# Kernel optimization log

Measured on AMD Instinct MI355X. Metric: run time of the kernel, lower is better.

## Reference

```python
import jax, jax.numpy as jnp
import numpy as np

B, N, K, C = 4, 4096, 32, 192  # batch, npoint, nsample, channels (C % 6 == 0)
EPS = 1e-5


def setup_inputs() -> dict:
    key = jax.random.key(0)
    ks = jax.random.split(key, 8)
    p = jax.random.normal(ks[0], (B, N, 3), jnp.float32)
    x = jax.random.normal(ks[1], (B, C, N), jnp.float32)
    idx = jax.random.randint(ks[2], (B, N, K), 0, N)  # ball-query neighbor ids
    W = jax.random.normal(ks[3], (C, C + 3), jnp.float32) * 0.05  # 1x1 conv weight
    gamma = 1.0 + 0.1 * jax.random.normal(ks[4], (C,), jnp.float32)
    beta = 0.1 * jax.random.normal(ks[5], (C,), jnp.float32)
    rmean = 0.1 * jax.random.normal(ks[6], (C,), jnp.float32)
    rvar = jax.random.uniform(ks[7], (C,), jnp.float32) + 0.5  # positive running var
    return dict(p=p, x=x, idx=idx, W=W, gamma=gamma, beta=beta, rmean=rmean, rvar=rvar)


def reference(p, x, idx, W, gamma, beta, rmean, rvar):
    # --- grouper: gather neighbors, relative coords ---
    pn = jax.vmap(lambda pp, ii: pp[ii])(p, idx)            # [B,N,K,3]
    dp = jnp.transpose(pn - p[:, :, None, :], (0, 3, 1, 2))  # [B,3,N,K]
    xj = jax.vmap(lambda xx, ii: xx[:, ii])(x, idx)          # [B,C,N,K]
    # --- PosPool sin/cos positional embedding fused with features ---
    feat_dim = C // 6
    dim_mat = jnp.power(500.0, jnp.arange(feat_dim, dtype=jnp.float32) / feat_dim)
    div = (50.0 * dp)[..., None] / dim_mat                   # [B,3,N,K,fd]
    pe = jnp.concatenate([jnp.sin(div), jnp.cos(div)], axis=-1)  # [B,3,N,K,2fd]
    pe = jnp.transpose(pe, (0, 1, 4, 2, 3)).reshape(B, C, N, K)  # [B,C,N,K]
    agg = xj * pe + pe
    # --- dp_fj concat -> 1x1 conv -> BN(eval) -> ReLU ---
    h = jnp.concatenate([dp, agg], axis=1)                   # [B,C+3,N,K]
    y = jnp.einsum('oc,bcnk->bonk', W, h)                    # [B,C,N,K]
    inv = gamma / jnp.sqrt(rvar + EPS)
    y = y * inv[:, None, None] + (beta - rmean * inv)[:, None, None]
    y = jax.nn.relu(y)
    # --- max reduction over neighbors ---
    return jnp.max(y, axis=-1)                               # [B,C,N]
```

## Files before the change

kernel.cpp:

```cpp
#include <hip/hip_runtime.h>
#include <math.h>

#define B_   4
#define N_   4096
#define K_   32
#define C_   192
#define CH_  195
#define KPAD 224
#define NKT6 6
#define NNT8 8
#define GRID 512

using half8  = __attribute__((ext_vector_type(8))) _Float16;
using half2v = __attribute__((ext_vector_type(2))) _Float16;
using f32x4  = __attribute__((ext_vector_type(4))) float;

__device__ _Float16 g_Wp[C_ * KPAD];
__device__ _Float16 g_xT[(size_t)B_ * N_ * C_];

__global__ __launch_bounds__(256) void prep(const float* __restrict__ x,
                                            const float* __restrict__ W,
                                            const float* __restrict__ gamma_,
                                            const float* __restrict__ rvar) {
    const int tid = threadIdx.x;
    if (blockIdx.x < 512) {
        __shared__ float s[32][201];
        const int b  = blockIdx.x >> 7;
        const int n0 = (blockIdx.x & 127) * 32;
        const int cl = tid >> 3;
        const int n4 = (tid & 7) * 4;
#pragma unroll
        for (int it = 0; it < 6; ++it) {
            const int c = it * 32 + cl;
            const float4 v = *(const float4*)(x + ((size_t)b * C_ + c) * N_ + n0 + n4);
            s[n4 + 0][c] = v.x; s[n4 + 1][c] = v.y; s[n4 + 2][c] = v.z; s[n4 + 3][c] = v.w;
        }
        __syncthreads();
        const int n  = tid >> 3;
        const int og = tid & 7;
#pragma unroll
        for (int it = 0; it < 3; ++it) {
            const int oc = it * 8 + og;
            half8 v;
#pragma unroll
            for (int jj = 0; jj < 8; ++jj) v[jj] = (_Float16)s[n][oc * 8 + jj];
            *(half8*)(g_xT + ((size_t)b * N_ + n0 + n) * C_ + oc * 8) = v;
        }
    } else {
        const int i = (blockIdx.x - 512) * 256 + tid;
        if (i < C_ * KPAD) {
            const int o = i / KPAD, r = i - o * KPAD;
            const float inv = gamma_[o] * rsqrtf(rvar[o] + 1e-5f);
            float v = 0.0f;
            if (r < 192)      v = W[o * CH_ + 3 + r];
            else if (r < 195) v = W[o * CH_ + (r - 192)];
            g_Wp[i] = (_Float16)(v * inv);
        }
    }
}

__global__ __launch_bounds__(256, 2) void la_mfma(
    const float* __restrict__ p,
    const int*   __restrict__ idx,
    const float* __restrict__ gamma_,
    const float* __restrict__ beta_,
    const float* __restrict__ rmean,
    const float* __restrict__ rvar,
    float* __restrict__ out)
{
    __shared__ _Float16 hb[NKT6 * NNT8 * 64 * 8];
    __shared__ float s_d[3][128];
    __shared__ float s_bias[C_], s_fr[32];

    const int tid  = threadIdx.x;
    const int lane = tid & 63;
    const int w    = tid >> 6;
    const int l15  = lane & 15;
    const int quad = lane >> 4;

    const int xcd      = blockIdx.x & 7;
    const int slot     = blockIdx.x >> 3;
    const int pairbase = xcd * 1024 + slot * 16;
    const int iters    = 8;
    const int b        = xcd >> 1;

    if (tid < C_) {
        const float inv = gamma_[tid] * rsqrtf(rvar[tid] + 1e-5f);
        s_bias[tid] = beta_[tid] - rmean[tid] * inv;
    }
    if (tid < 32) s_fr[tid] = 7.9577471546f * exp2f(-(float)tid * 0.2801808715263400f);
    __syncthreads();

    float sfr[8];
#pragma unroll
    for (int jj = 0; jj < 8; ++jj) sfr[jj] = s_fr[quad * 8 + jj];

    const int pt = w >> 1;
    const int k  = (w & 1) * 16 + l15;

    int j0 = idx[(size_t)((pairbase + 0) * 2 + pt) * K_ + k];
    int j1 = idx[(size_t)((pairbase + 1) * 2 + pt) * K_ + k];

    for (int it = 0; it < iters; ++it) {
        const int pr0 = pairbase + 2 * it;
        const int n0  = (pr0 * 2) & (N_ - 1);

#pragma unroll
        for (int pp = 0; pp < 2; ++pp) {
            const int j  = pp ? j1 : j0;
            const int gp = (pr0 + pp) * 2 + pt;
            const float d0 = p[(size_t)(b * N_ + j) * 3 + 0] - p[(size_t)gp * 3 + 0];
            const float d1 = p[(size_t)(b * N_ + j) * 3 + 1] - p[(size_t)gp * 3 + 1];
            const float d2 = p[(size_t)(b * N_ + j) * 3 + 2] - p[(size_t)gp * 3 + 2];
            const _Float16* xh = g_xT + ((size_t)b * N_ + j) * C_;
            const int nt = pp * 4 + w;

#pragma unroll
            for (int i6 = 0; i6 < 6; ++i6) {
                const int chunk = quad + 4 * i6;
                const half8 v = *(const half8*)(xh + chunk * 8);
                const float dd  = (chunk < 8) ? d0 : ((chunk < 16) ? d1 : d2);
                const float off = (chunk & 4) ? 0.25f : 0.0f;
                half8 hv;
#pragma unroll
                for (int jj = 0; jj < 8; jj += 2) {
                    const float pe0 = __builtin_amdgcn_sinf(fmaf(dd, sfr[jj],     off));
                    const float pe1 = __builtin_amdgcn_sinf(fmaf(dd, sfr[jj + 1], off));
                    const half2v pe2 = __builtin_bit_cast(half2v, __builtin_amdgcn_cvt_pkrtz(pe0, pe1));
                    half2v v2; v2[0] = v[jj]; v2[1] = v[jj + 1];
                    const half2v r2 = pe2 * v2 + pe2;
                    hv[jj] = r2[0]; hv[jj + 1] = r2[1];
                }
                *(half8*)(&hb[(size_t)((i6 * NNT8 + nt) * 64 + quad * 16 + l15) * 8]) = hv;
            }
            if (quad == 0) {
                const int col = nt * 16 + l15;
                s_d[0][col] = d0; s_d[1][col] = d1; s_d[2][col] = d2;
            }
        }
        __syncthreads();

        if (it + 1 < iters) {
            j0 = idx[(size_t)((pr0 + 2) * 2 + pt) * K_ + k];
            j1 = idx[(size_t)((pr0 + 3) * 2 + pt) * K_ + k];
        }

        f32x4 acc[3][8];
#pragma unroll
        for (int i = 0; i < 3; ++i)
#pragma unroll
            for (int t = 0; t < 8; ++t) acc[i][t] = (f32x4)0.0f;

#pragma unroll
        for (int kt = 0; kt < NKT6; ++kt) {
            const int k0 = kt * 32 + quad * 8;
            half8 a[3];
#pragma unroll
            for (int i = 0; i < 3; ++i)
                a[i] = *(const half8*)(g_Wp + (size_t)((w * 3 + i) * 16 + l15) * KPAD + k0);
#pragma unroll
            for (int t = 0; t < 8; ++t) {
                const half8 bf = *(const half8*)(&hb[(size_t)((kt * NNT8 + t) * 64 + lane) * 8]);
#pragma unroll
                for (int i = 0; i < 3; ++i)
                    acc[i][t] = __builtin_amdgcn_mfma_f32_16x16x32_f16(bf, a[i], acc[i][t], 0, 0, 0);
            }
        }
        {
            half8 a6[3];
#pragma unroll
            for (int i = 0; i < 3; ++i)
                a6[i] = *(const half8*)(g_Wp + (size_t)((w * 3 + i) * 16 + l15) * KPAD + 6 * 32 + quad * 8);
#pragma unroll
            for (int t = 0; t < 8; ++t) {
                const int col = t * 16 + l15;
                half8 b6 = (half8)(_Float16)0.0f;
                const float e0 = s_d[0][col];
                const float e1 = s_d[1][col];
                const float e2 = s_d[2][col];
                if (quad == 0) {
                    b6[0] = (_Float16)e0; b6[1] = (_Float16)e1; b6[2] = (_Float16)e2;
                }
#pragma unroll
                for (int i = 0; i < 3; ++i)
                    acc[i][t] = __builtin_amdgcn_mfma_f32_16x16x32_f16(b6, a6[i], acc[i][t], 0, 0, 0);
            }
        }

#pragma unroll
        for (int i = 0; i < 3; ++i) {
            const int m = (w * 3 + i) * 16 + l15;
            float4 o4;
            float ov[4];
#pragma unroll
            for (int pp = 0; pp < 2; ++pp)
#pragma unroll
                for (int ptc = 0; ptc < 2; ++ptc) {
                    const f32x4 va = acc[i][pp * 4 + 2 * ptc];
                    const f32x4 vb = acc[i][pp * 4 + 2 * ptc + 1];
                    float v = fmaxf(fmaxf(fmaxf(va[0], va[1]), fmaxf(va[2], va[3])),
                                    fmaxf(fmaxf(vb[0], vb[1]), fmaxf(vb[2], vb[3])));
                    v = fmaxf(v, __shfl_xor(v, 16, 64));
                    v = fmaxf(v, __shfl_xor(v, 32, 64));
                    ov[pp * 2 + ptc] = v;
                }
            if (quad == 0) {
                const float bias = s_bias[m];
                o4.x = fmaxf(ov[0] + bias, 0.0f);
                o4.y = fmaxf(ov[1] + bias, 0.0f);
                o4.z = fmaxf(ov[2] + bias, 0.0f);
                o4.w = fmaxf(ov[3] + bias, 0.0f);
                *(float4*)(&out[((size_t)b * C_ + m) * N_ + n0]) = o4;
            }
        }
        __syncthreads();
    }
}

extern "C" void kernel_launch(void* const* d_in, const int* in_sizes, int n_in,
                              void* d_out, int out_size, void* d_ws, size_t ws_size,
                              hipStream_t stream) {
    (void)in_sizes; (void)n_in; (void)out_size; (void)d_ws; (void)ws_size;
    const float* p      = (const float*)d_in[0];
    const float* x      = (const float*)d_in[1];
    const int*   idx    = (const int*)d_in[2];
    const float* W      = (const float*)d_in[3];
    const float* gamma_ = (const float*)d_in[4];
    const float* beta_  = (const float*)d_in[5];
    const float* rmean  = (const float*)d_in[6];
    const float* rvar   = (const float*)d_in[7];
    float* out = (float*)d_out;

    prep<<<512 + (C_ * KPAD + 255) / 256, 256, 0, stream>>>(x, W, gamma_, rvar);
    la_mfma<<<GRID, 256, 0, stream>>>(p, idx, gamma_, beta_, rmean, rvar, out);
}
```

Before: 149.1 us.

## Double block size to 512 threads and stage outputs in LDS for wider stores

Each block now uses 8 waves over 8 points per iteration (16 N-tiles), with the grid halved to 256 blocks. Waves split into row groups and tile halves, so each weight fragment load serves the same number of MFMAs per wave but the block covers twice the points. Results are staged in a shared s_out buffer across two iterations and then written as 16 contiguous floats per channel row, replacing scattered 4-float stores. This costs more LDS, an extra barrier per iteration, and fewer blocks, which may lower occupancy and latency hiding.

```diff
diff --git a/kernel.cpp b/kernel.cpp
--- a/kernel.cpp
+++ b/kernel.cpp
@@ -8,8 +8,8 @@
 #define CH_  195
 #define KPAD 224
 #define NKT6 6
-#define NNT8 8
-#define GRID 512
+#define NNT16 16
+#define GRID 256
 
 using half8  = __attribute__((ext_vector_type(8))) _Float16;
 using half2v = __attribute__((ext_vector_type(2))) _Float16;
@@ -59,7 +59,7 @@
     }
 }
 
-__global__ __launch_bounds__(256, 2) void la_mfma(
+__global__ __launch_bounds__(512, 2) void la_mfma(
     const float* __restrict__ p,
     const int*   __restrict__ idx,
     const float* __restrict__ gamma_,
@@ -68,8 +68,9 @@
     const float* __restrict__ rvar,
     float* __restrict__ out)
 {
-    __shared__ _Float16 hb[NKT6 * NNT8 * 64 * 8];
-    __shared__ float s_d[3][128];
+    __shared__ _Float16 hb[7 * NNT16 * 64 * 8];
+    __shared__ float s_d[3][256];
+    __shared__ float s_out[C_][16];
     __shared__ float s_bias[C_], s_fr[32];
 
     const int tid  = threadIdx.x;
@@ -80,7 +81,7 @@
 
     const int xcd      = blockIdx.x & 7;
     const int slot     = blockIdx.x >> 3;
-    const int pairbase = xcd * 1024 + slot * 16;
+    const int pairbase = xcd * 1024 + slot * 32;
     const int iters    = 8;
     const int b        = xcd >> 1;
 
@@ -95,26 +96,22 @@
 #pragma unroll
     for (int jj = 0; jj < 8; ++jj) sfr[jj] = s_fr[quad * 8 + jj];
 
-    const int pt = w >> 1;
-    const int k  = (w & 1) * 16 + l15;
-
-    int j0 = idx[(size_t)((pairbase + 0) * 2 + pt) * K_ + k];
-    int j1 = idx[(size_t)((pairbase + 1) * 2 + pt) * K_ + k];
+    const int k0v = (w & 1) * 16 + l15;
+    const int pp0 = w >> 2,        pt0 = (w >> 1) & 1;
+    const int pp1 = (8 + w) >> 2,  pt1 = ((8 + w) >> 1) & 1;
+
+    int j0 = idx[(size_t)((pairbase + pp0) * 2 + pt0) * K_ + k0v];
+    int j1 = idx[(size_t)((pairbase + pp1) * 2 + pt1) * K_ + k0v];
 
     for (int it = 0; it < iters; ++it) {
-        const int pr0 = pairbase + 2 * it;
-        const int n0  = (pr0 * 2) & (N_ - 1);
-
-#pragma unroll
-        for (int pp = 0; pp < 2; ++pp) {
-            const int j  = pp ? j1 : j0;
+        const int pr0 = pairbase + 4 * it;
+
+        auto build = [&](int T, int jv, int pp, int pt) {
             const int gp = (pr0 + pp) * 2 + pt;
-            const float d0 = p[(size_t)(b * N_ + j) * 3 + 0] - p[(size_t)gp * 3 + 0];
-            const float d1 = p[(size_t)(b * N_ + j) * 3 + 1] - p[(size_t)gp * 3 + 1];
-            const float d2 = p[(size_t)(b * N_ + j) * 3 + 2] - p[(size_t)gp * 3 + 2];
-            const _Float16* xh = g_xT + ((size_t)b * N_ + j) * C_;
-            const int nt = pp * 4 + w;
-
+            const float d0 = p[(size_t)(b * N_ + jv) * 3 + 0] - p[(size_t)gp * 3 + 0];
+            const float d1 = p[(size_t)(b * N_ + jv) * 3 + 1] - p[(size_t)gp * 3 + 1];
+            const float d2 = p[(size_t)(b * N_ + jv) * 3 + 2] - p[(size_t)gp * 3 + 2];
+            const _Float16* xh = g_xT + ((size_t)b * N_ + jv) * C_;
 #pragma unroll
             for (int i6 = 0; i6 < 6; ++i6) {
                 const int chunk = quad + 4 * i6;
@@ -131,20 +128,25 @@
                     const half2v r2 = pe2 * v2 + pe2;
                     hv[jj] = r2[0]; hv[jj + 1] = r2[1];
                 }
-                *(half8*)(&hb[(size_t)((i6 * NNT8 + nt) * 64 + quad * 16 + l15) * 8]) = hv;
+                *(half8*)(&hb[(size_t)((i6 * NNT16 + T) * 64 + quad * 16 + l15) * 8]) = hv;
             }
             if (quad == 0) {
-                const int col = nt * 16 + l15;
+                const int col = T * 16 + l15;
                 s_d[0][col] = d0; s_d[1][col] = d1; s_d[2][col] = d2;
             }
-        }
+        };
+        build(w,     j0, pp0, pt0);
+        build(8 + w, j1, pp1, pt1);
         __syncthreads();
 
+        int jn0 = j0, jn1 = j1;
         if (it + 1 < iters) {
-            j0 = idx[(size_t)((pr0 + 2) * 2 + pt) * K_ + k];
-            j1 = idx[(size_t)((pr0 + 3) * 2 + pt) * K_ + k];
-        }
-
+            jn0 = idx[(size_t)((pr0 + 4 + pp0) * 2 + pt0) * K_ + k0v];
+            jn1 = idx[(size_t)((pr0 + 4 + pp1) * 2 + pt1) * K_ + k0v];
+        }
+
+        const int rg = (w & 3) * 3;
+        const int tb = (w >> 2) * 8;
         f32x4 acc[3][8];
 #pragma unroll
         for (int i = 0; i < 3; ++i)
@@ -153,27 +155,27 @@
 
 #pragma unroll
         for (int kt = 0; kt < NKT6; ++kt) {
-            const int k0 = kt * 32 + quad * 8;
+            const int kk0 = kt * 32 + quad * 8;
             half8 a[3];
 #pragma unroll
             for (int i = 0; i < 3; ++i)
-                a[i] = *(const half8*)(g_Wp + (size_t)((w * 3 + i) * 16 + l15) * KPAD + k0);
-#pragma unroll
-            for (int t = 0; t < 8; ++t) {
-                const half8 bf = *(const half8*)(&hb[(size_t)((kt * NNT8 + t) * 64 + lane) * 8]);
+                a[i] = *(const half8*)(g_Wp + (size_t)((rg + i) * 16 + l15) * KPAD + kk0);
+#pragma unroll
+            for (int tt = 0; tt < 8; ++tt) {
+                const half8 bf = *(const half8*)(&hb[(size_t)((kt * NNT16 + tb + tt) * 64 + lane) * 8]);
 #pragma unroll
                 for (int i = 0; i < 3; ++i)
-                    acc[i][t] = __builtin_amdgcn_mfma_f32_16x16x32_f16(bf, a[i], acc[i][t], 0, 0, 0);
+                    acc[i][tt] = __builtin_amdgcn_mfma_f32_16x16x32_f16(bf, a[i], acc[i][tt], 0, 0, 0);
             }
         }
         {
             half8 a6[3];
 #pragma unroll
             for (int i = 0; i < 3; ++i)
-                a6[i] = *(const half8*)(g_Wp + (size_t)((w * 3 + i) * 16 + l15) * KPAD + 6 * 32 + quad * 8);
-#pragma unroll
-            for (int t = 0; t < 8; ++t) {
-                const int col = t * 16 + l15;
+                a6[i] = *(const half8*)(g_Wp + (size_t)((rg + i) * 16 + l15) * KPAD + 6 * 32 + quad * 8);
+#pragma unroll
+            for (int tt = 0; tt < 8; ++tt) {
+                const int col = (tb + tt) * 16 + l15;
                 half8 b6 = (half8)(_Float16)0.0f;
                 const float e0 = s_d[0][col];
                 const float e1 = s_d[1][col];
@@ -183,37 +185,42 @@
                 }
 #pragma unroll
                 for (int i = 0; i < 3; ++i)
-                    acc[i][t] = __builtin_amdgcn_mfma_f32_16x16x32_f16(b6, a6[i], acc[i][t], 0, 0, 0);
-            }
-        }
-
+                    acc[i][tt] = __builtin_amdgcn_mfma_f32_16x16x32_f16(b6, a6[i], acc[i][tt], 0, 0, 0);
+            }
+        }
+
+        const int pbase = (it & 1) * 8 + (w >> 2) * 4;
 #pragma unroll
         for (int i = 0; i < 3; ++i) {
-            const int m = (w * 3 + i) * 16 + l15;
-            float4 o4;
-            float ov[4];
-#pragma unroll
-            for (int pp = 0; pp < 2; ++pp)
-#pragma unroll
-                for (int ptc = 0; ptc < 2; ++ptc) {
-                    const f32x4 va = acc[i][pp * 4 + 2 * ptc];
-                    const f32x4 vb = acc[i][pp * 4 + 2 * ptc + 1];
-                    float v = fmaxf(fmaxf(fmaxf(va[0], va[1]), fmaxf(va[2], va[3])),
-                                    fmaxf(fmaxf(vb[0], vb[1]), fmaxf(vb[2], vb[3])));
-                    v = fmaxf(v, __shfl_xor(v, 16, 64));
-                    v = fmaxf(v, __shfl_xor(v, 32, 64));
-                    ov[pp * 2 + ptc] = v;
+            const int m = (rg + i) * 16 + l15;
+#pragma unroll
+            for (int qq = 0; qq < 4; ++qq) {
+                const f32x4 va = acc[i][2 * qq];
+                const f32x4 vb = acc[i][2 * qq + 1];
+                float v = fmaxf(fmaxf(fmaxf(va[0], va[1]), fmaxf(va[2], va[3])),
+                                fmaxf(fmaxf(vb[0], vb[1]), fmaxf(vb[2], vb[3])));
+                v = fmaxf(v, __shfl_xor(v, 16, 64));
+                v = fmaxf(v, __shfl_xor(v, 32, 64));
+                if (quad == 0)
+                    s_out[m][pbase + qq] = fmaxf(v + s_bias[m], 0.0f);
+            }
+        }
+        __syncthreads();
+
+        if (it & 1) {
+            const int n0w = ((pr0 - 4) * 2) & (N_ - 1);
+#pragma unroll
+            for (int ss = 0; ss < 2; ++ss) {
+                const int t = ss * 512 + tid;
+                if (t < C_ * 4) {
+                    const int row = t >> 2, c4 = (t & 3) * 4;
+                    const float4 o4 = *(const float4*)(&s_out[row][c4]);
+                    *(float4*)(&out[((size_t)b * C_ + row) * N_ + n0w + c4]) = o4;
                 }
-            if (quad == 0) {
-                const float bias = s_bias[m];
-                o4.x = fmaxf(ov[0] + bias, 0.0f);
-                o4.y = fmaxf(ov[1] + bias, 0.0f);
-                o4.z = fmaxf(ov[2] + bias, 0.0f);
-                o4.w = fmaxf(ov[3] + bias, 0.0f);
-                *(float4*)(&out[((size_t)b * C_ + m) * N_ + n0]) = o4;
-            }
-        }
-        __syncthreads();
+            }
+        }
+
+        j0 = jn0; j1 = jn1;
     }
 }
 
@@ -232,5 +239,5 @@
     float* out = (float*)d_out;
 
     prep<<<512 + (C_ * KPAD + 255) / 256, 256, 0, stream>>>(x, W, gamma_, rvar);
-    la_mfma<<<GRID, 256, 0, stream>>>(p, idx, gamma_, beta_, rmean, rvar, out);
+    la_mfma<<<GRID, 512, 0, stream>>>(p, idx, gamma_, beta_, rmean, rvar, out);
 }
```

After: 157.2 us. 5.4% more time.

## Double block size to 512 threads, splitting gather and MFMA tiles across eight waves

Applied to the files above, without the earlier changes.

Each block now runs eight waves instead of four. Each wave gathers and builds the positional-embedding tile for one point pair, and in the GEMM each wave handles three output row groups over four neighbor tiles instead of eight. This halves per-wave accumulator registers and raises the number of resident waves, so more gather latency can be hidden. The cost is that W fragments are reloaded by twice as many waves, and output stores shrink to float2.

```diff
diff --git a/kernel.cpp b/kernel.cpp
--- a/kernel.cpp
+++ b/kernel.cpp
@@ -59,7 +59,7 @@
     }
 }
 
-__global__ __launch_bounds__(256, 2) void la_mfma(
+__global__ __launch_bounds__(512, 4) void la_mfma(
     const float* __restrict__ p,
     const int*   __restrict__ idx,
     const float* __restrict__ gamma_,
@@ -95,26 +95,22 @@
 #pragma unroll
     for (int jj = 0; jj < 8; ++jj) sfr[jj] = s_fr[quad * 8 + jj];
 
-    const int pt = w >> 1;
-    const int k  = (w & 1) * 16 + l15;
-
-    int j0 = idx[(size_t)((pairbase + 0) * 2 + pt) * K_ + k];
-    int j1 = idx[(size_t)((pairbase + 1) * 2 + pt) * K_ + k];
+    const int pp = w >> 2;
+    const int pt = (w >> 1) & 1;
+    const int kk = (w & 1) * 16 + l15;
+
+    int j = idx[(size_t)((pairbase + pp) * 2 + pt) * K_ + kk];
 
     for (int it = 0; it < iters; ++it) {
         const int pr0 = pairbase + 2 * it;
         const int n0  = (pr0 * 2) & (N_ - 1);
 
-#pragma unroll
-        for (int pp = 0; pp < 2; ++pp) {
-            const int j  = pp ? j1 : j0;
+        {
             const int gp = (pr0 + pp) * 2 + pt;
             const float d0 = p[(size_t)(b * N_ + j) * 3 + 0] - p[(size_t)gp * 3 + 0];
             const float d1 = p[(size_t)(b * N_ + j) * 3 + 1] - p[(size_t)gp * 3 + 1];
             const float d2 = p[(size_t)(b * N_ + j) * 3 + 2] - p[(size_t)gp * 3 + 2];
             const _Float16* xh = g_xT + ((size_t)b * N_ + j) * C_;
-            const int nt = pp * 4 + w;
-
 #pragma unroll
             for (int i6 = 0; i6 < 6; ++i6) {
                 const int chunk = quad + 4 * i6;
@@ -131,49 +127,49 @@
                     const half2v r2 = pe2 * v2 + pe2;
                     hv[jj] = r2[0]; hv[jj + 1] = r2[1];
                 }
-                *(half8*)(&hb[(size_t)((i6 * NNT8 + nt) * 64 + quad * 16 + l15) * 8]) = hv;
+                *(half8*)(&hb[(size_t)((i6 * NNT8 + w) * 64 + quad * 16 + l15) * 8]) = hv;
             }
             if (quad == 0) {
-                const int col = nt * 16 + l15;
+                const int col = w * 16 + l15;
                 s_d[0][col] = d0; s_d[1][col] = d1; s_d[2][col] = d2;
             }
         }
         __syncthreads();
 
-        if (it + 1 < iters) {
-            j0 = idx[(size_t)((pr0 + 2) * 2 + pt) * K_ + k];
-            j1 = idx[(size_t)((pr0 + 3) * 2 + pt) * K_ + k];
-        }
-
-        f32x4 acc[3][8];
+        if (it + 1 < iters)
+            j = idx[(size_t)((pr0 + 2 + pp) * 2 + pt) * K_ + kk];
+
+        const int rg = (w & 3) * 3;
+        const int tb = (w >> 2) * 4;
+        f32x4 acc[3][4];
 #pragma unroll
         for (int i = 0; i < 3; ++i)
 #pragma unroll
-            for (int t = 0; t < 8; ++t) acc[i][t] = (f32x4)0.0f;
+            for (int t = 0; t < 4; ++t) acc[i][t] = (f32x4)0.0f;
 
 #pragma unroll
         for (int kt = 0; kt < NKT6; ++kt) {
-            const int k0 = kt * 32 + quad * 8;
+            const int kk0 = kt * 32 + quad * 8;
             half8 a[3];
 #pragma unroll
             for (int i = 0; i < 3; ++i)
-                a[i] = *(const half8*)(g_Wp + (size_t)((w * 3 + i) * 16 + l15) * KPAD + k0);
-#pragma unroll
-            for (int t = 0; t < 8; ++t) {
-                const half8 bf = *(const half8*)(&hb[(size_t)((kt * NNT8 + t) * 64 + lane) * 8]);
+                a[i] = *(const half8*)(g_Wp + (size_t)((rg + i) * 16 + l15) * KPAD + kk0);
+#pragma unroll
+            for (int tt = 0; tt < 4; ++tt) {
+                const half8 bf = *(const half8*)(&hb[(size_t)((kt * NNT8 + tb + tt) * 64 + lane) * 8]);
 #pragma unroll
                 for (int i = 0; i < 3; ++i)
-                    acc[i][t] = __builtin_amdgcn_mfma_f32_16x16x32_f16(bf, a[i], acc[i][t], 0, 0, 0);
+                    acc[i][tt] = __builtin_amdgcn_mfma_f32_16x16x32_f16(bf, a[i], acc[i][tt], 0, 0, 0);
             }
         }
         {
             half8 a6[3];
 #pragma unroll
             for (int i = 0; i < 3; ++i)
-                a6[i] = *(const half8*)(g_Wp + (size_t)((w * 3 + i) * 16 + l15) * KPAD + 6 * 32 + quad * 8);
-#pragma unroll
-            for (int t = 0; t < 8; ++t) {
-                const int col = t * 16 + l15;
+                a6[i] = *(const half8*)(g_Wp + (size_t)((rg + i) * 16 + l15) * KPAD + 6 * 32 + quad * 8);
+#pragma unroll
+            for (int tt = 0; tt < 4; ++tt) {
+                const int col = (tb + tt) * 16 + l15;
                 half8 b6 = (half8)(_Float16)0.0f;
                 const float e0 = s_d[0][col];
                 const float e1 = s_d[1][col];
@@ -183,34 +179,30 @@
                 }
 #pragma unroll
                 for (int i = 0; i < 3; ++i)
-                    acc[i][t] = __builtin_amdgcn_mfma_f32_16x16x32_f16(b6, a6[i], acc[i][t], 0, 0, 0);
+                    acc[i][tt] = __builtin_amdgcn_mfma_f32_16x16x32_f16(b6, a6[i], acc[i][tt], 0, 0, 0);
             }
         }
 
 #pragma unroll
         for (int i = 0; i < 3; ++i) {
-            const int m = (w * 3 + i) * 16 + l15;
-            float4 o4;
-            float ov[4];
-#pragma unroll
-            for (int pp = 0; pp < 2; ++pp)
-#pragma unroll
-                for (int ptc = 0; ptc < 2; ++ptc) {
-                    const f32x4 va = acc[i][pp * 4 + 2 * ptc];
-                    const f32x4 vb = acc[i][pp * 4 + 2 * ptc + 1];
-                    float v = fmaxf(fmaxf(fmaxf(va[0], va[1]), fmaxf(va[2], va[3])),
-                                    fmaxf(fmaxf(vb[0], vb[1]), fmaxf(vb[2], vb[3])));
-                    v = fmaxf(v, __shfl_xor(v, 16, 64));
-                    v = fmaxf(v, __shfl_xor(v, 32, 64));
-                    ov[pp * 2 + ptc] = v;
-                }
+            const int m = (rg + i) * 16 + l15;
+            float vv[2];
+#pragma unroll
+            for (int P = 0; P < 2; ++P) {
+                const f32x4 va = acc[i][2 * P];
+                const f32x4 vb = acc[i][2 * P + 1];
+                float v = fmaxf(fmaxf(fmaxf(va[0], va[1]), fmaxf(va[2], va[3])),
+                                fmaxf(fmaxf(vb[0], vb[1]), fmaxf(vb[2], vb[3])));
+                v = fmaxf(v, __shfl_xor(v, 16, 64));
+                v = fmaxf(v, __shfl_xor(v, 32, 64));
+                vv[P] = v;
+            }
             if (quad == 0) {
                 const float bias = s_bias[m];
-                o4.x = fmaxf(ov[0] + bias, 0.0f);
-                o4.y = fmaxf(ov[1] + bias, 0.0f);
-                o4.z = fmaxf(ov[2] + bias, 0.0f);
-                o4.w = fmaxf(ov[3] + bias, 0.0f);
-                *(float4*)(&out[((size_t)b * C_ + m) * N_ + n0]) = o4;
+                float2 o2;
+                o2.x = fmaxf(vv[0] + bias, 0.0f);
+                o2.y = fmaxf(vv[1] + bias, 0.0f);
+                *(float2*)(&out[((size_t)b * C_ + m) * N_ + n0 + (w >> 2) * 2]) = o2;
             }
         }
         __syncthreads();
@@ -232,5 +224,5 @@
     float* out = (float*)d_out;
 
     prep<<<512 + (C_ * KPAD + 255) / 256, 256, 0, stream>>>(x, W, gamma_, rvar);
-    la_mfma<<<GRID, 256, 0, stream>>>(p, idx, gamma_, beta_, rmean, rvar, out);
+    la_mfma<<<GRID, 512, 0, stream>>>(p, idx, gamma_, beta_, rmean, rvar, out);
 }
```

Result: slower. 179.9 us (+20.7%).

## Fuse prep into main kernel with a device-wide atomic grid barrier

Applied to the files above, without the earlier changes.

The separate prep kernel (x transpose to half precision and folding the BN scale into the weights) is merged into the main MFMA kernel. Each block first does its share of the prep work, reusing the feature shared buffer for the transpose, then waits at a software grid barrier built from an atomic counter before starting the main computation. This removes one kernel launch and the gap between the two kernels. In exchange it relies on all 512 blocks being resident at once (256 threads, two blocks per CU) and adds barrier spin time.

```diff
diff --git a/kernel.cpp b/kernel.cpp
--- a/kernel.cpp
+++ b/kernel.cpp
@@ -17,69 +17,82 @@
 
 __device__ _Float16 g_Wp[C_ * KPAD];
 __device__ _Float16 g_xT[(size_t)B_ * N_ * C_];
-
-__global__ __launch_bounds__(256) void prep(const float* __restrict__ x,
-                                            const float* __restrict__ W,
-                                            const float* __restrict__ gamma_,
-                                            const float* __restrict__ rvar) {
-    const int tid = threadIdx.x;
-    if (blockIdx.x < 512) {
-        __shared__ float s[32][201];
-        const int b  = blockIdx.x >> 7;
-        const int n0 = (blockIdx.x & 127) * 32;
-        const int cl = tid >> 3;
-        const int n4 = (tid & 7) * 4;
-#pragma unroll
-        for (int it = 0; it < 6; ++it) {
-            const int c = it * 32 + cl;
-            const float4 v = *(const float4*)(x + ((size_t)b * C_ + c) * N_ + n0 + n4);
-            s[n4 + 0][c] = v.x; s[n4 + 1][c] = v.y; s[n4 + 2][c] = v.z; s[n4 + 3][c] = v.w;
-        }
-        __syncthreads();
-        const int n  = tid >> 3;
-        const int og = tid & 7;
-#pragma unroll
-        for (int it = 0; it < 3; ++it) {
-            const int oc = it * 8 + og;
-            half8 v;
-#pragma unroll
-            for (int jj = 0; jj < 8; ++jj) v[jj] = (_Float16)s[n][oc * 8 + jj];
-            *(half8*)(g_xT + ((size_t)b * N_ + n0 + n) * C_ + oc * 8) = v;
-        }
-    } else {
-        const int i = (blockIdx.x - 512) * 256 + tid;
-        if (i < C_ * KPAD) {
-            const int o = i / KPAD, r = i - o * KPAD;
-            const float inv = gamma_[o] * rsqrtf(rvar[o] + 1e-5f);
-            float v = 0.0f;
-            if (r < 192)      v = W[o * CH_ + 3 + r];
-            else if (r < 195) v = W[o * CH_ + (r - 192)];
-            g_Wp[i] = (_Float16)(v * inv);
-        }
-    }
-}
-
-__global__ __launch_bounds__(256, 2) void la_mfma(
+__device__ unsigned int g_ctr;
+
+__global__ __launch_bounds__(256, 2) void la_fused(
     const float* __restrict__ p,
+    const float* __restrict__ x,
     const int*   __restrict__ idx,
+    const float* __restrict__ W,
     const float* __restrict__ gamma_,
     const float* __restrict__ beta_,
     const float* __restrict__ rmean,
     const float* __restrict__ rvar,
     float* __restrict__ out)
 {
-    __shared__ _Float16 hb[NKT6 * NNT8 * 64 * 8];
+    __shared__ unsigned char s_raw[49152];
     __shared__ float s_d[3][128];
     __shared__ float s_bias[C_], s_fr[32];
+
+    _Float16* hb = (_Float16*)s_raw;
+    float (*ts)[201] = (float(*)[201])s_raw;
 
     const int tid  = threadIdx.x;
     const int lane = tid & 63;
     const int w    = tid >> 6;
     const int l15  = lane & 15;
     const int quad = lane >> 4;
-
-    const int xcd      = blockIdx.x & 7;
-    const int slot     = blockIdx.x >> 3;
+    const int bid  = blockIdx.x;
+
+    if (bid < 168) {
+        const int i = bid * 256 + tid;
+        const int o = i / KPAD, r = i - o * KPAD;
+        const float inv = gamma_[o] * rsqrtf(rvar[o] + 1e-5f);
+        float v = 0.0f;
+        if (r < 192)      v = W[o * CH_ + 3 + r];
+        else if (r < 195) v = W[o * CH_ + (r - 192)];
+        g_Wp[i] = (_Float16)(v * inv);
+    }
+    {
+        const int tb = bid >> 7;
+        const int n0 = (bid & 127) * 32;
+        const int cl = tid >> 3;
+        const int n4 = (tid & 7) * 4;
+#pragma unroll
+        for (int it = 0; it < 6; ++it) {
+            const int c = it * 32 + cl;
+            const float4 v = *(const float4*)(x + ((size_t)tb * C_ + c) * N_ + n0 + n4);
+            ts[n4 + 0][c] = v.x; ts[n4 + 1][c] = v.y; ts[n4 + 2][c] = v.z; ts[n4 + 3][c] = v.w;
+        }
+        __syncthreads();
+        const int n  = tid >> 3;
+        const int og = tid & 7;
+#pragma unroll
+        for (int it = 0; it < 3; ++it) {
+            const int oc = it * 8 + og;
+            half8 v;
+#pragma unroll
+            for (int jj = 0; jj < 8; ++jj) v[jj] = (_Float16)ts[n][oc * 8 + jj];
+            *(half8*)(g_xT + ((size_t)tb * N_ + n0 + n) * C_ + oc * 8) = v;
+        }
+    }
+
+    __syncthreads();
+    if (tid == 0) {
+        __threadfence();
+        const unsigned a = __hip_atomic_fetch_add(&g_ctr, 1u, __ATOMIC_ACQ_REL,
+                                                  __HIP_MEMORY_SCOPE_AGENT);
+        const unsigned target = (a / (unsigned)GRID + 1u) * (unsigned)GRID;
+        while (__hip_atomic_load(&g_ctr, __ATOMIC_ACQUIRE,
+                                 __HIP_MEMORY_SCOPE_AGENT) < target) {
+            __builtin_amdgcn_s_sleep(2);
+        }
+        __threadfence();
+    }
+    __syncthreads();
+
+    const int xcd      = bid & 7;
+    const int slot     = bid >> 3;
     const int pairbase = xcd * 1024 + slot * 16;
     const int iters    = 8;
     const int b        = xcd >> 1;
@@ -231,6 +244,5 @@
     const float* rvar   = (const float*)d_in[7];
     float* out = (float*)d_out;
 
-    prep<<<512 + (C_ * KPAD + 255) / 256, 256, 0, stream>>>(x, W, gamma_, rvar);
-    la_mfma<<<GRID, 256, 0, stream>>>(p, idx, gamma_, beta_, rmean, rvar, out);
+    la_fused<<<GRID, 256, 0, stream>>>(p, x, idx, W, gamma_, beta_, rmean, rvar, out);
 }
```

Result: slower. 211.4 us (+41.8%).
